# Performance work log

Measured on AMD Instinct MI355X. Metric: run time of the kernel, lower is better.

The kernel has to match this reference:

```python
import jax, jax.numpy as jnp
import numpy as np

EPS = 1e-5

def adain_norm(x):
    # per-(batch,channel) instance normalization over spatial dims (AdaIN projection)
    mean = jnp.mean(x, axis=(2, 3), keepdims=True)
    var = jnp.var(x, axis=(2, 3), keepdims=True)
    return (x - mean) / jnp.sqrt(var + EPS)

def conv1x1(x, w, b):
    # x: [B,C,H,W], w: [O,C], b: [O]
    return jnp.einsum('bchw,oc->bohw', x, w) + b[None, :, None, None]

def setup_inputs() -> dict:
    key = jax.random.key(0)
    ks = jax.random.split(key, 10)
    B, C, H, W = 4, 512, 64, 64
    s = 1.0 / np.sqrt(C)
    return {
        'x': jax.random.normal(ks[0], (B, C, H, W), jnp.float32),
        'y': jax.random.normal(ks[1], (B, C, H, W), jnp.float32),
        'f_w': jax.random.normal(ks[2], (C, C), jnp.float32) * s,
        'f_b': jnp.zeros((C,), jnp.float32),
        'g_w': jax.random.normal(ks[3], (C, C), jnp.float32) * s,
        'g_b': jnp.zeros((C,), jnp.float32),
        'h_w': jax.random.normal(ks[4], (C, C), jnp.float32) * s,
        'h_b': jnp.zeros((C,), jnp.float32),
        'out_w': jax.random.normal(ks[5], (C, C), jnp.float32) * s,
        'out_b': jnp.zeros((C,), jnp.float32),
    }

def reference(x, y, f_w, f_b, g_w, g_b, h_w, h_b, out_w, out_b):
    B, C, H, W = x.shape
    HW = H * W
    xn = adain_norm(x)
    yn = adain_norm(y)
    # 1x1 conv projections, flattened over spatial dims
    f = conv1x1(xn, f_w, f_b).reshape(B, C, HW)   # [B,C,HWx]
    g = conv1x1(yn, g_w, g_b).reshape(B, C, HW)   # [B,C,HWy]
    energy = jnp.einsum('bci,bcj->bij', f, g)     # [B,HWx,HWy]
    correlation = jax.nn.softmax(energy, axis=-1)
    h = conv1x1(y, h_w, h_b).reshape(B, C, HW)    # [B,C,HWy]
    # residual = h @ correlation^T -> [B,C,HWx]
    residual = jnp.einsum('bcj,bij->bci', h, correlation).reshape(B, C, H, W)
    residual = conv1x1(residual, out_w, out_b)
    return x + residual
```

## Files before the change

### kernel.cpp

```cpp
#include <hip/hip_runtime.h>
#include <stdint.h>

#define HW 4096
#define NC 512
#define NB 4

typedef __attribute__((ext_vector_type(8))) _Float16 f16x8;
typedef __attribute__((ext_vector_type(4))) float f32x4;
typedef __attribute__((ext_vector_type(4))) unsigned short ush4;
typedef __attribute__((ext_vector_type(8))) unsigned short ush8;

typedef __attribute__((address_space(1))) const void* as1_cvp;
typedef __attribute__((address_space(3))) void* as3_vp;

__device__ __forceinline__ unsigned short f2h(float f) {
  union { _Float16 h; unsigned short u; } c;
  c.h = (_Float16)f;
  return c.u;
}
__device__ __forceinline__ float h2f(unsigned short u) {
  union { unsigned short u; _Float16 h; } c;
  c.u = u;
  return (float)c.h;
}

__global__ __launch_bounds__(256) void moments_k(const float* __restrict__ x,
                                                 const float* __restrict__ y,
                                                 float* __restrict__ stats) {
  int bid = blockIdx.x;
  int tens = bid >> 11;
  int row = bid & 2047;
  const float* src = (tens ? y : x) + (size_t)row * HW;
  float s = 0.f, s2 = 0.f;
  for (int j = threadIdx.x; j < HW / 4; j += 256) {
    float4 v = ((const float4*)src)[j];
    s += (v.x + v.y) + (v.z + v.w);
    s2 += (v.x * v.x + v.y * v.y) + (v.z * v.z + v.w * v.w);
  }
  #pragma unroll
  for (int o = 32; o; o >>= 1) { s += __shfl_down(s, o); s2 += __shfl_down(s2, o); }
  __shared__ float rs[8];
  int w = threadIdx.x >> 6;
  if ((threadIdx.x & 63) == 0) { rs[w] = s; rs[4 + w] = s2; }
  __syncthreads();
  if (threadIdx.x == 0) {
    float S = (rs[0] + rs[1]) + (rs[2] + rs[3]);
    float S2 = (rs[4] + rs[5]) + (rs[6] + rs[7]);
    float mean = S * (1.f / HW);
    float var = S2 * (1.f / HW) - mean * mean;
    stats[tens * 4096 + row] = mean;
    stats[tens * 4096 + 2048 + row] = rsqrtf(var + 1e-5f);
  }
}

__global__ __launch_bounds__(256) void transnorm_k(const float* __restrict__ x,
                                                   const float* __restrict__ y,
                                                   const float* __restrict__ stats,
                                                   unsigned short* __restrict__ xnT,
                                                   unsigned short* __restrict__ ynT,
                                                   unsigned short* __restrict__ yH) {
  __shared__ float tile[64][65];
  __shared__ float ms[64], rsd[64];
  int zi = blockIdx.z;
  int b = zi >> 1, mode = zi & 1;
  int i0 = blockIdx.x * 64, c0 = blockIdx.y * 64;
  const float* src = mode ? y : x;
  int t = threadIdx.x;
  int c = t >> 2;
  int isub = (t & 3) << 4;
  if (t < 64) {
    int srow = (mode ? 4096 : 0) + b * NC + c0 + t;
    ms[t] = stats[srow];
    rsd[t] = stats[srow + 2048];
  }
  const float4* sp = (const float4*)(src + ((size_t)(b * NC + c0 + c)) * HW + i0 + isub);
  #pragma unroll
  for (int k = 0; k < 4; ++k) {
    float4 v = sp[k];
    int ib = isub + k * 4;
    tile[ib + 0][c] = v.x;
    tile[ib + 1][c] = v.y;
    tile[ib + 2][c] = v.z;
    tile[ib + 3][c] = v.w;
    if (mode) {
      ush4 yo;
      yo[0] = f2h(v.x); yo[1] = f2h(v.y); yo[2] = f2h(v.z); yo[3] = f2h(v.w);
      *(ush4*)(yH + ((size_t)(b * NC + c0 + c)) * HW + i0 + isub + k * 4) = yo;
    }
  }
  __syncthreads();
  int i = t >> 2;
  int cc = (t & 3) << 4;
  size_t obase = ((size_t)b * HW + i0 + i) * NC + c0 + cc;
  unsigned short* dst = mode ? ynT : xnT;
  #pragma unroll
  for (int h = 0; h < 2; ++h) {
    ush8 o;
    #pragma unroll
    for (int e = 0; e < 8; ++e) {
      int ce = cc + h * 8 + e;
      o[e] = f2h((tile[i][ce] - ms[ce]) * rsd[ce]);
    }
    *(ush8*)(dst + obase + h * 8) = o;
  }
}

__global__ __launch_bounds__(256) void castw_k(const float* __restrict__ fw,
                                               const float* __restrict__ gw,
                                               const float* __restrict__ hw_,
                                               const float* __restrict__ ow,
                                               unsigned short* __restrict__ fwT,
                                               unsigned short* __restrict__ gwT,
                                               unsigned short* __restrict__ hwT,
                                               unsigned short* __restrict__ owB) {
  __shared__ float tile[64][65];
  int which = blockIdx.z;
  const float* src = which == 0 ? fw : which == 1 ? gw : which == 2 ? hw_ : ow;
  unsigned short* dst = which == 0 ? fwT : which == 1 ? gwT : which == 2 ? hwT : owB;
  int r0 = blockIdx.x * 64, c0 = blockIdx.y * 64;
  int t = threadIdx.x;
  int r = t >> 2;
  int csub = (t & 3) << 4;
  const float4* sp = (const float4*)(src + (size_t)(r0 + r) * 512 + c0 + csub);
  if (which == 3) {
    #pragma unroll
    for (int k = 0; k < 4; ++k) {
      float4 v = sp[k];
      ush4 o;
      o[0] = f2h(v.x); o[1] = f2h(v.y); o[2] = f2h(v.z); o[3] = f2h(v.w);
      *(ush4*)(dst + (size_t)(r0 + r) * 512 + c0 + csub + k * 4) = o;
    }
    return;
  }
  #pragma unroll
  for (int k = 0; k < 4; ++k) {
    float4 v = sp[k];
    int cb = csub + k * 4;
    tile[cb + 0][r] = v.x;
    tile[cb + 1][r] = v.y;
    tile[cb + 2][r] = v.z;
    tile[cb + 3][r] = v.w;
  }
  __syncthreads();
  int cw = t >> 2;
  int rsub = (t & 3) << 4;
  #pragma unroll
  for (int h = 0; h < 2; ++h) {
    ush8 o;
    #pragma unroll
    for (int e = 0; e < 8; ++e) o[e] = f2h(tile[cw][rsub + h * 8 + e]);
    *(ush8*)(dst + (size_t)(c0 + cw) * 512 + r0 + rsub + h * 8) = o;
  }
}

__global__ __launch_bounds__(256) void dotrows_h(const unsigned short* __restrict__ A,
                                                 const float* __restrict__ vec,
                                                 float* __restrict__ out) {
  int row = blockIdx.x * 4 + (threadIdx.x >> 6);
  int lane = threadIdx.x & 63;
  ush8 a = *(const ush8*)(A + (size_t)row * 512 + lane * 8);
  float s = 0.f;
  #pragma unroll
  for (int e = 0; e < 8; ++e) s += h2f(a[e]) * vec[lane * 8 + e];
  #pragma unroll
  for (int o = 32; o; o >>= 1) s += __shfl_down(s, o);
  if (lane == 0) out[row] = s;
}

__global__ __launch_bounds__(256) void b2_k(const float* __restrict__ Wf,
                                            const float* __restrict__ hb,
                                            const float* __restrict__ ob,
                                            float* __restrict__ out) {
  int row = blockIdx.x * 4 + (threadIdx.x >> 6);
  int lane = threadIdx.x & 63;
  const float4* a = (const float4*)(Wf + (size_t)row * 512) + lane * 2;
  float4 x0 = a[0], x1 = a[1];
  const float4* hv = (const float4*)hb + lane * 2;
  float4 h0 = hv[0], h1 = hv[1];
  float s = x0.x * h0.x + x0.y * h0.y + x0.z * h0.z + x0.w * h0.w
          + x1.x * h1.x + x1.y * h1.y + x1.z * h1.z + x1.w * h1.w;
  #pragma unroll
  for (int o = 32; o; o >>= 1) s += __shfl_down(s, o);
  if (lane == 0) out[row] = ob[row] + s;
}

__global__ __launch_bounds__(256) void softmax_h(unsigned short* __restrict__ S) {
  unsigned short* row = S + (size_t)blockIdx.x * HW;
  int t = threadIdx.x;
  ush8 a0 = *(const ush8*)(row + t * 16);
  ush8 a1 = *(const ush8*)(row + t * 16 + 8);
  float v[16];
  #pragma unroll
  for (int e = 0; e < 8; ++e) { v[e] = h2f(a0[e]); v[8 + e] = h2f(a1[e]); }
  float mx = -3.0e38f;
  #pragma unroll
  for (int e = 0; e < 16; ++e) mx = fmaxf(mx, v[e]);
  #pragma unroll
  for (int o = 32; o; o >>= 1) mx = fmaxf(mx, __shfl_down(mx, o));
  __shared__ float red[8];
  int w = t >> 6;
  if ((t & 63) == 0) red[w] = mx;
  __syncthreads();
  mx = fmaxf(fmaxf(red[0], red[1]), fmaxf(red[2], red[3]));
  float sum = 0.f;
  #pragma unroll
  for (int e = 0; e < 16; ++e) { v[e] = __expf(v[e] - mx); sum += v[e]; }
  #pragma unroll
  for (int o = 32; o; o >>= 1) sum += __shfl_down(sum, o);
  if ((t & 63) == 0) red[4 + w] = sum;
  __syncthreads();
  float inv = 1.f / ((red[4] + red[5]) + (red[6] + red[7]));
  ush8 o0, o1;
  #pragma unroll
  for (int e = 0; e < 8; ++e) { o0[e] = f2h(v[e] * inv); o1[e] = f2h(v[8 + e] * inv); }
  *(ush8*)(row + t * 16) = o0;
  *(ush8*)(row + t * 16 + 8) = o1;
}

__global__ __launch_bounds__(256) void reduce_k(const float* __restrict__ P4,
                                                unsigned short* __restrict__ op,
                                                long long PSo, int R, int pzs) {
  int e = blockIdx.x * 256 + threadIdx.x;
  int bg = e >> pzs;
  int rem = e - (bg << pzs);
  const float4* base = (const float4*)P4 + ((size_t)bg * 4) * R * (NC / 4) + rem;
  float4 s = {0.f, 0.f, 0.f, 0.f};
  #pragma unroll
  for (int sp = 0; sp < 4; ++sp) {
    float4 v = base[(size_t)sp * R * (NC / 4)];
    s.x += v.x; s.y += v.y; s.z += v.z; s.w += v.w;
  }
  int m = rem >> 7, c4 = rem & 127;
  ush4 o;
  o[0] = f2h(s.x); o[1] = f2h(s.y); o[2] = f2h(s.z); o[3] = f2h(s.w);
  *(ush4*)(op + (size_t)bg * PSo + (size_t)m * NC + c4 * 4) = o;
}

__global__ __launch_bounds__(256, 2) void gemm_ntp(
    const unsigned short* __restrict__ A, long long sA, int lda,
    const unsigned short* __restrict__ Bm, long long sB, int ldb,
    void* __restrict__ Cp, long long sC, long long sCs, int ldc,
    int K, int out_f32, int ls,
    const float* __restrict__ bias_m, const float* __restrict__ bias_n,
    const float* __restrict__ add_src, long long sAdd,
    const unsigned short* __restrict__ B2, const float* __restrict__ bias_n2,
    int zsw) {
  __shared__ short lsA[2][128 * 64];
  __shared__ short lsB[2][128 * 64];
  const int t = threadIdx.x;
  const int lane = t & 63;
  const int w = t >> 6;
  const int wm = w >> 1, wn = w & 1;
  const long long bz = blockIdx.z;
  if ((int)bz >= zsw) { Bm = B2; bias_n = bias_n2; }
  const long long bg = bz >> ls;
  const int sp = (int)(bz - (bg << ls));
  const long long koff = (long long)sp * K;
  const unsigned short* Ab = A + bz * sA * (ls ? 0 : 1) + (ls ? bg * sA : 0) + koff
                           + (size_t)blockIdx.x * 128 * lda;
  const unsigned short* Bb = Bm + bg * sB + koff + (size_t)blockIdx.y * 128 * ldb;

  f32x4 zero = {0.f, 0.f, 0.f, 0.f};
  f32x4 acc[4][4];
  #pragma unroll
  for (int i = 0; i < 4; ++i)
    #pragma unroll
    for (int j = 0; j < 4; ++j) acc[i][j] = zero;

  const int nkt = K >> 6;

  auto STAGE = [&](int buf, int kt) {
    const int kbase = kt << 6;
    #pragma unroll
    for (int i = 0; i < 4; ++i) {
      int q = t + i * 256;
      int r = q >> 3, xx = q & 7;
      int gk = kbase + ((xx ^ (r & 7)) << 3);
      __builtin_amdgcn_global_load_lds((as1_cvp)(const void*)(Ab + (size_t)r * lda + gk),
                                       (as3_vp)(void*)(&lsA[buf][q << 3]), 16, 0, 0);
      __builtin_amdgcn_global_load_lds((as1_cvp)(const void*)(Bb + (size_t)r * ldb + gk),
                                       (as3_vp)(void*)(&lsB[buf][q << 3]), 16, 0, 0);
    }
  };

  STAGE(0, 0);
  __syncthreads();
  int cur = 0;
  for (int kt = 0; kt < nkt; ++kt) {
    if (kt + 1 < nkt) STAGE(cur ^ 1, kt + 1);
    #pragma unroll
    for (int ks = 0; ks < 2; ++ks) {
      f16x8 av[4], bv[4];
      const int xl = ks * 4 + (lane >> 4);
      const int rr = lane & 15;
      #pragma unroll
      for (int mb = 0; mb < 4; ++mb) {
        int row = wm * 64 + mb * 16 + rr;
        av[mb] = *(const f16x8*)&lsA[cur][(row << 6) + ((xl ^ (row & 7)) << 3)];
      }
      #pragma unroll
      for (int nb = 0; nb < 4; ++nb) {
        int row = wn * 64 + nb * 16 + rr;
        bv[nb] = *(const f16x8*)&lsB[cur][(row << 6) + ((xl ^ (row & 7)) << 3)];
      }
      __builtin_amdgcn_s_setprio(1);
      #pragma unroll
      for (int mb = 0; mb < 4; ++mb)
        #pragma unroll
        for (int nb = 0; nb < 4; ++nb)
          acc[mb][nb] = __builtin_amdgcn_mfma_f32_16x16x32_f16(av[mb], bv[nb], acc[mb][nb], 0, 0, 0);
      __builtin_amdgcn_s_setprio(0);
    }
    __syncthreads();
    cur ^= 1;
  }

  const int mb0 = blockIdx.x * 128 + wm * 64;
  const int nb0 = blockIdx.y * 128 + wn * 64;
  const int cn = lane & 15;
  const int rq = (lane >> 4) << 2;
  float* cf = (float*)Cp;
  unsigned short* ch = (unsigned short*)Cp;
  #pragma unroll
  for (int mb = 0; mb < 4; ++mb) {
    #pragma unroll
    for (int nb = 0; nb < 4; ++nb) {
      int n = nb0 + nb * 16 + cn;
      float bn = bias_n ? bias_n[n] : 0.f;
      #pragma unroll
      for (int r = 0; r < 4; ++r) {
        int m = mb0 + mb * 16 + rq + r;
        float vv = acc[mb][nb][r] + bn;
        if (bias_m) vv += bias_m[m];
        if (add_src) vv += add_src[bg * sAdd + (size_t)m * ldc + n];
        size_t off = (size_t)(bg * sC) + (size_t)sp * sCs + (size_t)m * ldc + n;
        if (out_f32) cf[off] = vv;
        else ch[off] = f2h(vv);
      }
    }
  }
}

__global__ __launch_bounds__(512, 2) void gemm_nt2(
    const unsigned short* __restrict__ A, long long sA, int lda,
    const unsigned short* __restrict__ Bm, long long sB, int ldb,
    void* __restrict__ Cp, long long sC, int ldc,
    int K, int out_f32,
    const float* __restrict__ bias_n, long long sBn) {
  __shared__ short lsA[2][256 * 64];
  __shared__ short lsB[2][256 * 64];
  const int t = threadIdx.x;
  const int lane = t & 63;
  const int w = t >> 6;
  const int wm = w >> 2, wn = w & 3;
  const long long bz = blockIdx.z;
  const unsigned short* Ab = A + bz * sA + (size_t)blockIdx.x * 256 * lda;
  const unsigned short* Bb = Bm + bz * sB + (size_t)blockIdx.y * 256 * ldb;

  f32x4 zero = {0.f, 0.f, 0.f, 0.f};
  f32x4 acc[8][4];
  #pragma unroll
  for (int i = 0; i < 8; ++i)
    #pragma unroll
    for (int j = 0; j < 4; ++j) acc[i][j] = zero;

  const int rr = lane & 15;
  const int xl = lane >> 4;
  const int nkt = K >> 6;

  auto STAGE = [&](int buf, int kt) {
    const int kbase = kt << 6;
    #pragma unroll
    for (int i = 0; i < 4; ++i) {
      int q = t + i * 512;
      int r = q >> 3, xx = q & 7;
      int gk = kbase + ((xx ^ (r & 7)) << 3);
      __builtin_amdgcn_global_load_lds((as1_cvp)(const void*)(Ab + (size_t)r * lda + gk),
                                       (as3_vp)(void*)(&lsA[buf][q << 3]), 16, 0, 0);
      __builtin_amdgcn_global_load_lds((as1_cvp)(const void*)(Bb + (size_t)r * ldb + gk),
                                       (as3_vp)(void*)(&lsB[buf][q << 3]), 16, 0, 0);
    }
  };

  STAGE(0, 0);
  __syncthreads();
  int cur = 0;
  for (int kt = 0; kt < nkt; ++kt) {
    if (kt + 1 < nkt) STAGE(cur ^ 1, kt + 1);
    #pragma unroll
    for (int ks = 0; ks < 2; ++ks) {
      f16x8 av[8], bv[4];
      const int cb = ks * 4 + xl;
      #pragma unroll
      for (int mb = 0; mb < 8; ++mb) {
        int row = wm * 128 + mb * 16 + rr;
        av[mb] = *(const f16x8*)&lsA[cur][(row << 6) + ((cb ^ (row & 7)) << 3)];
      }
      #pragma unroll
      for (int nb = 0; nb < 4; ++nb) {
        int row = wn * 64 + nb * 16 + rr;
        bv[nb] = *(const f16x8*)&lsB[cur][(row << 6) + ((cb ^ (row & 7)) << 3)];
      }
      __builtin_amdgcn_s_setprio(1);
      #pragma unroll
      for (int mb = 0; mb < 8; ++mb)
        #pragma unroll
        for (int nb = 0; nb < 4; ++nb)
          acc[mb][nb] = __builtin_amdgcn_mfma_f32_16x16x32_f16(av[mb], bv[nb], acc[mb][nb], 0, 0, 0);
      __builtin_amdgcn_s_setprio(0);
    }
    __syncthreads();
    cur ^= 1;
  }

  const int mb0 = blockIdx.x * 256 + wm * 128;
  const int nb0 = blockIdx.y * 256 + wn * 64;
  const int cn = lane & 15;
  const int rq = (lane >> 4) << 2;
  float* cf = (float*)Cp;
  unsigned short* ch = (unsigned short*)Cp;
  #pragma unroll
  for (int mb = 0; mb < 8; ++mb) {
    #pragma unroll
    for (int nb = 0; nb < 4; ++nb) {
      int n = nb0 + nb * 16 + cn;
      float bn = bias_n ? bias_n[bz * sBn + n] : 0.f;
      #pragma unroll
      for (int r = 0; r < 4; ++r) {
        int m = mb0 + mb * 16 + rq + r;
        float vv = acc[mb][nb][r] + bn;
        size_t off = (size_t)(bz * sC) + (size_t)m * ldc + n;
        if (out_f32) cf[off] = vv;
        else ch[off] = f2h(vv);
      }
    }
  }
}

extern "C" void kernel_launch(void* const* d_in, const int* in_sizes, int n_in,
                              void* d_out, int out_size, void* d_ws, size_t ws_size,
                              hipStream_t stream) {
  const float* x = (const float*)d_in[0];
  const float* y = (const float*)d_in[1];
  const float* f_w = (const float*)d_in[2];
  const float* f_b = (const float*)d_in[3];
  const float* g_w = (const float*)d_in[4];
  const float* g_b = (const float*)d_in[5];
  const float* h_w = (const float*)d_in[6];
  const float* h_b = (const float*)d_in[7];
  const float* out_w = (const float*)d_in[8];
  const float* out_b = (const float*)d_in[9];
  float* out = (float*)d_out;
  (void)g_b;

  char* ws = (char*)d_ws;
  size_t off = 0;
  auto alloc = [&](size_t bytes) -> char* {
    char* p = ws + off;
    off += (bytes + 255) & ~(size_t)255;
    return p;
  };
  const size_t TN = (size_t)NB * HW * NC;
  const size_t WN = (size_t)512 * 512;
  float* stats = (float*)alloc(8192 * sizeof(float));
  unsigned short* fwT = (unsigned short*)alloc(WN * 2);
  unsigned short* gwT = (unsigned short*)alloc(WN * 2);
  unsigned short* hwT = (unsigned short*)alloc(WN * 2);
  unsigned short* owB = (unsigned short*)alloc(WN * 2);
  unsigned short* W1T = (unsigned short*)alloc(WN * 2);
  unsigned short* W2 = (unsigned short*)alloc(WN * 2);
  float* vv = (float*)alloc(512 * 4);
  float* b2 = (float*)alloc(512 * 4);
  float* wj = (float*)alloc((size_t)NB * HW * 4);
  unsigned short* xnT = (unsigned short*)alloc(TN * 2);
  unsigned short* ynT = (unsigned short*)alloc(TN * 2);
  unsigned short* yH = (unsigned short*)alloc(TN * 2);
  unsigned short* fB = (unsigned short*)alloc(TN * 2);
  unsigned short* oB = xnT;
  size_t remain = ws_size > off ? ws_size - off : 0;
  const size_t SB = (size_t)HW * HW * 2 + (size_t)4 * HW * NC * 4;
  int G, R = HW;
  if (remain >= 4 * SB)      { G = 4; }
  else if (remain >= 2 * SB) { G = 2; }
  else if (remain >= SB)     { G = 1; }
  else {
    G = 1;
    while (R > 128 && (size_t)R * (HW * 2 + 16 * NC) > remain) R >>= 1;
  }
  unsigned short* Sh = (unsigned short*)alloc((size_t)G * R * HW * 2);
  float* P4 = (float*)alloc((size_t)G * 4 * R * NC * 4);
  if (off > ws_size) return;

  const long long PS = (long long)HW * NC;
  const int BIG = 1 << 30;

  castw_k<<<dim3(8, 8, 4), dim3(256), 0, stream>>>(f_w, g_w, h_w, out_w,
                                                   fwT, gwT, hwT, owB);
  moments_k<<<dim3(4096), dim3(256), 0, stream>>>(x, y, stats);
  transnorm_k<<<dim3(64, 8, 8), dim3(256), 0, stream>>>(x, y, stats, xnT, ynT, yH);

  dotrows_h<<<dim3(128), dim3(256), 0, stream>>>(gwT, f_b, vv);
  b2_k<<<dim3(128), dim3(256), 0, stream>>>(out_w, h_b, out_b, b2);
  gemm_ntp<<<dim3(4, 4, 1), dim3(256), 0, stream>>>(
      gwT, 0, 512, fwT, 0, 512, W1T, 0, 0, 512, 512, 0, 0,
      nullptr, nullptr, nullptr, 0, nullptr, nullptr, BIG);
  gemm_ntp<<<dim3(4, 4, 1), dim3(256), 0, stream>>>(
      owB, 0, 512, hwT, 0, 512, W2, 0, 0, 512, 512, 0, 0,
      nullptr, nullptr, nullptr, 0, nullptr, nullptr, BIG);
  dotrows_h<<<dim3(NB * HW / 4), dim3(256), 0, stream>>>(ynT, vv, wj);
  gemm_ntp<<<dim3(32, 4, NB), dim3(256), 0, stream>>>(
      xnT, PS, NC, W1T, 0, NC, fB, PS, 0, NC, NC, 0, 0,
      nullptr, nullptr, nullptr, 0, nullptr, nullptr, BIG);

  const int pzs = 31 - __builtin_clz((unsigned)(R * (NC / 4)));
  for (int b0 = 0; b0 < NB; b0 += G) {
    for (int r0 = 0; r0 < HW; r0 += R) {
      if (R >= 256) {
        gemm_nt2<<<dim3(R / 256, HW / 256, G), dim3(512), 0, stream>>>(
            fB + ((size_t)b0 * HW + r0) * NC, PS, NC,
            ynT + (size_t)b0 * PS, PS, NC,
            Sh, (long long)R * HW, HW, NC, 0,
            wj + (size_t)b0 * HW, HW);
      } else {
        gemm_ntp<<<dim3(R / 128, 32, G), dim3(256), 0, stream>>>(
            fB + ((size_t)b0 * HW + r0) * NC, PS, NC,
            ynT + (size_t)b0 * PS, PS, NC,
            Sh, (long long)R * HW, 0, HW, NC, 0, 0,
            nullptr, wj + (size_t)b0 * HW, nullptr, 0, nullptr, nullptr, BIG);
      }
      softmax_h<<<dim3(G * R), dim3(256), 0, stream>>>(Sh);
      gemm_ntp<<<dim3(R / 128, 4, G * 4), dim3(256), 0, stream>>>(
          Sh, (long long)R * HW, HW,
          yH + (size_t)b0 * NC * HW, (long long)NC * HW, HW,
          P4, (long long)4 * R * NC, (long long)R * NC, NC, HW / 4, 1, 2,
          nullptr, nullptr, nullptr, 0, nullptr, nullptr, BIG);
      reduce_k<<<dim3(G * R / 2), dim3(256), 0, stream>>>(
          P4, oB + ((size_t)b0 * HW + r0) * NC, PS, R, pzs);
    }
  }
  gemm_ntp<<<dim3(4, 32, NB), dim3(256), 0, stream>>>(
      W2, 0, NC, oB, PS, NC,
      out, (long long)NC * HW, 0, HW, NC, 1, 0,
      b2, nullptr, x, (long long)NC * HW, nullptr, nullptr, BIG);
}
```

Before: 407.2 us.

## Deepen big-GEMM pipeline to four stages and reuse it for split-K PV GEMM

The 256x256 GEMM kernel moves from a double-buffered BK=64 loop to a 4-slot BK=32 ring, with three tiles in flight. Each step now waits on a partial vmcnt and a raw s_barrier instead of a full __syncthreads, which is meant to hide global-load latency. The kernel also gains split-K batching (sp offset plus output stride), so the softmax-times-h GEMM can use this larger-tile kernel instead of the 128-tile gemm_ntp when R>=256. The price is more barriers per K, a changed swizzle, and correctness that depends on the hand-counted vmcnt values.

```diff
diff --git a/kernel.cpp b/kernel.cpp
--- a/kernel.cpp
+++ b/kernel.cpp
@@ -341,21 +341,24 @@
   }
 }
 
-__global__ __launch_bounds__(512, 2) void gemm_nt2(
+__global__ __launch_bounds__(512, 2) void gemm_ntq(
     const unsigned short* __restrict__ A, long long sA, int lda,
     const unsigned short* __restrict__ Bm, long long sB, int ldb,
-    void* __restrict__ Cp, long long sC, int ldc,
-    int K, int out_f32,
+    void* __restrict__ Cp, long long sC, long long sCs, int ldc,
+    int K, int out_f32, int ls,
     const float* __restrict__ bias_n, long long sBn) {
-  __shared__ short lsA[2][256 * 64];
-  __shared__ short lsB[2][256 * 64];
+  __shared__ short lsA[4][256 * 32];
+  __shared__ short lsB[4][256 * 32];
   const int t = threadIdx.x;
   const int lane = t & 63;
   const int w = t >> 6;
   const int wm = w >> 2, wn = w & 3;
   const long long bz = blockIdx.z;
-  const unsigned short* Ab = A + bz * sA + (size_t)blockIdx.x * 256 * lda;
-  const unsigned short* Bb = Bm + bz * sB + (size_t)blockIdx.y * 256 * ldb;
+  const long long bg = bz >> ls;
+  const int sp = (int)(bz - (bg << ls));
+  const long long koff = (long long)sp * K;
+  const unsigned short* Ab = A + bg * sA + koff + (size_t)blockIdx.x * 256 * lda;
+  const unsigned short* Bb = Bm + bg * sB + koff + (size_t)blockIdx.y * 256 * ldb;
 
   f32x4 zero = {0.f, 0.f, 0.f, 0.f};
   f32x4 acc[8][4];
@@ -366,52 +369,69 @@
 
   const int rr = lane & 15;
   const int xl = lane >> 4;
-  const int nkt = K >> 6;
-
-  auto STAGE = [&](int buf, int kt) {
-    const int kbase = kt << 6;
-    #pragma unroll
-    for (int i = 0; i < 4; ++i) {
+  const int nkt = K >> 5;
+
+  auto STAGE = [&](int kt) {
+    const int slot = kt & 3;
+    const int kbase = kt << 5;
+    #pragma unroll
+    for (int i = 0; i < 2; ++i) {
       int q = t + i * 512;
-      int r = q >> 3, xx = q & 7;
-      int gk = kbase + ((xx ^ (r & 7)) << 3);
+      int r = q >> 2, xx = q & 3;
+      int gk = kbase + ((xx ^ ((r >> 1) & 3)) << 3);
       __builtin_amdgcn_global_load_lds((as1_cvp)(const void*)(Ab + (size_t)r * lda + gk),
-                                       (as3_vp)(void*)(&lsA[buf][q << 3]), 16, 0, 0);
+                                       (as3_vp)(void*)(&lsA[slot][q << 3]), 16, 0, 0);
       __builtin_amdgcn_global_load_lds((as1_cvp)(const void*)(Bb + (size_t)r * ldb + gk),
-                                       (as3_vp)(void*)(&lsB[buf][q << 3]), 16, 0, 0);
+                                       (as3_vp)(void*)(&lsB[slot][q << 3]), 16, 0, 0);
     }
   };
 
-  STAGE(0, 0);
-  __syncthreads();
-  int cur = 0;
-  for (int kt = 0; kt < nkt; ++kt) {
-    if (kt + 1 < nkt) STAGE(cur ^ 1, kt + 1);
-    #pragma unroll
-    for (int ks = 0; ks < 2; ++ks) {
-      f16x8 av[8], bv[4];
-      const int cb = ks * 4 + xl;
+  auto COMPUTE = [&](int kt) {
+    const int slot = kt & 3;
+    f16x8 av[8], bv[4];
+    #pragma unroll
+    for (int mb = 0; mb < 8; ++mb) {
+      int row = wm * 128 + mb * 16 + rr;
+      av[mb] = *(const f16x8*)&lsA[slot][(row << 5) + ((xl ^ ((row >> 1) & 3)) << 3)];
+    }
+    #pragma unroll
+    for (int nb = 0; nb < 4; ++nb) {
+      int row = wn * 64 + nb * 16 + rr;
+      bv[nb] = *(const f16x8*)&lsB[slot][(row << 5) + ((xl ^ ((row >> 1) & 3)) << 3)];
+    }
+    __builtin_amdgcn_s_setprio(1);
+    #pragma unroll
+    for (int mb = 0; mb < 8; ++mb)
       #pragma unroll
-      for (int mb = 0; mb < 8; ++mb) {
-        int row = wm * 128 + mb * 16 + rr;
-        av[mb] = *(const f16x8*)&lsA[cur][(row << 6) + ((cb ^ (row & 7)) << 3)];
-      }
-      #pragma unroll
-      for (int nb = 0; nb < 4; ++nb) {
-        int row = wn * 64 + nb * 16 + rr;
-        bv[nb] = *(const f16x8*)&lsB[cur][(row << 6) + ((cb ^ (row & 7)) << 3)];
-      }
-      __builtin_amdgcn_s_setprio(1);
-      #pragma unroll
-      for (int mb = 0; mb < 8; ++mb)
-        #pragma unroll
-        for (int nb = 0; nb < 4; ++nb)
-          acc[mb][nb] = __builtin_amdgcn_mfma_f32_16x16x32_f16(av[mb], bv[nb], acc[mb][nb], 0, 0, 0);
-      __builtin_amdgcn_s_setprio(0);
-    }
-    __syncthreads();
-    cur ^= 1;
-  }
+      for (int nb = 0; nb < 4; ++nb)
+        acc[mb][nb] = __builtin_amdgcn_mfma_f32_16x16x32_f16(av[mb], bv[nb], acc[mb][nb], 0, 0, 0);
+    __builtin_amdgcn_s_setprio(0);
+  };
+
+  STAGE(0); STAGE(1); STAGE(2);
+  asm volatile("s_waitcnt vmcnt(8)" ::: "memory");
+  __builtin_amdgcn_s_barrier();
+  __builtin_amdgcn_sched_barrier(0);
+
+  int kt = 0;
+  for (; kt + 3 < nkt; ++kt) {
+    STAGE(kt + 3);
+    COMPUTE(kt);
+    asm volatile("s_waitcnt vmcnt(8)" ::: "memory");
+    __builtin_amdgcn_s_barrier();
+    __builtin_amdgcn_sched_barrier(0);
+  }
+  COMPUTE(kt);
+  asm volatile("s_waitcnt vmcnt(4)" ::: "memory");
+  __builtin_amdgcn_s_barrier();
+  __builtin_amdgcn_sched_barrier(0);
+  ++kt;
+  COMPUTE(kt);
+  asm volatile("s_waitcnt vmcnt(0)" ::: "memory");
+  __builtin_amdgcn_s_barrier();
+  __builtin_amdgcn_sched_barrier(0);
+  ++kt;
+  COMPUTE(kt);
 
   const int mb0 = blockIdx.x * 256 + wm * 128;
   const int nb0 = blockIdx.y * 256 + wn * 64;
@@ -424,12 +444,12 @@
     #pragma unroll
     for (int nb = 0; nb < 4; ++nb) {
       int n = nb0 + nb * 16 + cn;
-      float bn = bias_n ? bias_n[bz * sBn + n] : 0.f;
+      float bn = bias_n ? bias_n[bg * sBn + n] : 0.f;
       #pragma unroll
       for (int r = 0; r < 4; ++r) {
         int m = mb0 + mb * 16 + rq + r;
         float vv = acc[mb][nb][r] + bn;
-        size_t off = (size_t)(bz * sC) + (size_t)m * ldc + n;
+        size_t off = (size_t)(bg * sC) + (size_t)sp * sCs + (size_t)m * ldc + n;
         if (out_f32) cf[off] = vv;
         else ch[off] = f2h(vv);
       }
@@ -516,24 +536,30 @@
   for (int b0 = 0; b0 < NB; b0 += G) {
     for (int r0 = 0; r0 < HW; r0 += R) {
       if (R >= 256) {
-        gemm_nt2<<<dim3(R / 256, HW / 256, G), dim3(512), 0, stream>>>(
+        gemm_ntq<<<dim3(R / 256, HW / 256, G), dim3(512), 0, stream>>>(
             fB + ((size_t)b0 * HW + r0) * NC, PS, NC,
             ynT + (size_t)b0 * PS, PS, NC,
-            Sh, (long long)R * HW, HW, NC, 0,
+            Sh, (long long)R * HW, 0, HW, NC, 0, 0,
             wj + (size_t)b0 * HW, HW);
+        softmax_h<<<dim3(G * R), dim3(256), 0, stream>>>(Sh);
+        gemm_ntq<<<dim3(R / 256, NC / 256, G * 4), dim3(512), 0, stream>>>(
+            Sh, (long long)R * HW, HW,
+            yH + (size_t)b0 * NC * HW, (long long)NC * HW, HW,
+            P4, (long long)4 * R * NC, (long long)R * NC, NC, HW / 4, 1, 2,
+            nullptr, 0);
       } else {
         gemm_ntp<<<dim3(R / 128, 32, G), dim3(256), 0, stream>>>(
             fB + ((size_t)b0 * HW + r0) * NC, PS, NC,
             ynT + (size_t)b0 * PS, PS, NC,
             Sh, (long long)R * HW, 0, HW, NC, 0, 0,
             nullptr, wj + (size_t)b0 * HW, nullptr, 0, nullptr, nullptr, BIG);
+        softmax_h<<<dim3(G * R), dim3(256), 0, stream>>>(Sh);
+        gemm_ntp<<<dim3(R / 128, 4, G * 4), dim3(256), 0, stream>>>(
+            Sh, (long long)R * HW, HW,
+            yH + (size_t)b0 * NC * HW, (long long)NC * HW, HW,
+            P4, (long long)4 * R * NC, (long long)R * NC, NC, HW / 4, 1, 2,
+            nullptr, nullptr, nullptr, 0, nullptr, nullptr, BIG);
       }
-      softmax_h<<<dim3(G * R), dim3(256), 0, stream>>>(Sh);
-      gemm_ntp<<<dim3(R / 128, 4, G * 4), dim3(256), 0, stream>>>(
-          Sh, (long long)R * HW, HW,
-          yH + (size_t)b0 * NC * HW, (long long)NC * HW, HW,
-          P4, (long long)4 * R * NC, (long long)R * NC, NC, HW / 4, 1, 2,
-          nullptr, nullptr, nullptr, 0, nullptr, nullptr, BIG);
       reduce_k<<<dim3(G * R / 2), dim3(256), 0, stream>>>(
           P4, oB + ((size_t)b0 * HW + r0) * NC, PS, R, pzs);
     }
```

Result: slower. 438.4 us (+7.7%).

## Fold split-K partial sums into final GEMM via duplicated weight matrix

Applied to the files above, without the earlier changes.

The attention-value GEMM previously split K into 4 fp32 partial buffers, which a separate reduce kernel summed and cast to fp16. Now K is split in 2, each half is written as fp16 into a concatenated 1024-wide buffer, and the output projection GEMM runs over K=1024 with a weight matrix replicated twice. This removes the reduce kernel and its fp32 partial traffic, and halves the split so each block does more K work. The cost is double the K work in the final GEMM, fewer blocks in the AV GEMM, and fp16 rounding of partial sums.

```diff
diff --git a/kernel.cpp b/kernel.cpp
--- a/kernel.cpp
+++ b/kernel.cpp
@@ -153,6 +153,15 @@
   }
 }
 
+__global__ __launch_bounds__(256) void repl_k(const unsigned short* __restrict__ W2,
+                                              unsigned short* __restrict__ W2x2) {
+  int idx = blockIdx.x * 256 + threadIdx.x;
+  int o = idx >> 7;
+  int k = (idx & 127) * 8;
+  ush8 v = *(const ush8*)(W2 + (size_t)o * 512 + (k & 511));
+  *(ush8*)(W2x2 + (size_t)o * 1024 + k) = v;
+}
+
 __global__ __launch_bounds__(256) void dotrows_h(const unsigned short* __restrict__ A,
                                                  const float* __restrict__ vec,
                                                  float* __restrict__ out) {
@@ -215,25 +224,6 @@
   for (int e = 0; e < 8; ++e) { o0[e] = f2h(v[e] * inv); o1[e] = f2h(v[8 + e] * inv); }
   *(ush8*)(row + t * 16) = o0;
   *(ush8*)(row + t * 16 + 8) = o1;
-}
-
-__global__ __launch_bounds__(256) void reduce_k(const float* __restrict__ P4,
-                                                unsigned short* __restrict__ op,
-                                                long long PSo, int R, int pzs) {
-  int e = blockIdx.x * 256 + threadIdx.x;
-  int bg = e >> pzs;
-  int rem = e - (bg << pzs);
-  const float4* base = (const float4*)P4 + ((size_t)bg * 4) * R * (NC / 4) + rem;
-  float4 s = {0.f, 0.f, 0.f, 0.f};
-  #pragma unroll
-  for (int sp = 0; sp < 4; ++sp) {
-    float4 v = base[(size_t)sp * R * (NC / 4)];
-    s.x += v.x; s.y += v.y; s.z += v.z; s.w += v.w;
-  }
-  int m = rem >> 7, c4 = rem & 127;
-  ush4 o;
-  o[0] = f2h(s.x); o[1] = f2h(s.y); o[2] = f2h(s.z); o[3] = f2h(s.w);
-  *(ush4*)(op + (size_t)bg * PSo + (size_t)m * NC + c4 * 4) = o;
 }
 
 __global__ __launch_bounds__(256, 2) void gemm_ntp(
@@ -469,6 +459,7 @@
   unsigned short* owB = (unsigned short*)alloc(WN * 2);
   unsigned short* W1T = (unsigned short*)alloc(WN * 2);
   unsigned short* W2 = (unsigned short*)alloc(WN * 2);
+  unsigned short* W2x2 = (unsigned short*)alloc((size_t)512 * 1024 * 2);
   float* vv = (float*)alloc(512 * 4);
   float* b2 = (float*)alloc(512 * 4);
   float* wj = (float*)alloc((size_t)NB * HW * 4);
@@ -476,19 +467,18 @@
   unsigned short* ynT = (unsigned short*)alloc(TN * 2);
   unsigned short* yH = (unsigned short*)alloc(TN * 2);
   unsigned short* fB = (unsigned short*)alloc(TN * 2);
-  unsigned short* oB = xnT;
+  unsigned short* Zp = (unsigned short*)alloc((size_t)NB * HW * 1024 * 2);
   size_t remain = ws_size > off ? ws_size - off : 0;
-  const size_t SB = (size_t)HW * HW * 2 + (size_t)4 * HW * NC * 4;
+  const size_t SB = (size_t)HW * HW * 2;
   int G, R = HW;
   if (remain >= 4 * SB)      { G = 4; }
   else if (remain >= 2 * SB) { G = 2; }
   else if (remain >= SB)     { G = 1; }
   else {
     G = 1;
-    while (R > 128 && (size_t)R * (HW * 2 + 16 * NC) > remain) R >>= 1;
+    while (R > 128 && (size_t)R * HW * 2 > remain) R >>= 1;
   }
   unsigned short* Sh = (unsigned short*)alloc((size_t)G * R * HW * 2);
-  float* P4 = (float*)alloc((size_t)G * 4 * R * NC * 4);
   if (off > ws_size) return;
 
   const long long PS = (long long)HW * NC;
@@ -507,12 +497,12 @@
   gemm_ntp<<<dim3(4, 4, 1), dim3(256), 0, stream>>>(
       owB, 0, 512, hwT, 0, 512, W2, 0, 0, 512, 512, 0, 0,
       nullptr, nullptr, nullptr, 0, nullptr, nullptr, BIG);
+  repl_k<<<dim3(256), dim3(256), 0, stream>>>(W2, W2x2);
   dotrows_h<<<dim3(NB * HW / 4), dim3(256), 0, stream>>>(ynT, vv, wj);
   gemm_ntp<<<dim3(32, 4, NB), dim3(256), 0, stream>>>(
       xnT, PS, NC, W1T, 0, NC, fB, PS, 0, NC, NC, 0, 0,
       nullptr, nullptr, nullptr, 0, nullptr, nullptr, BIG);
 
-  const int pzs = 31 - __builtin_clz((unsigned)(R * (NC / 4)));
   for (int b0 = 0; b0 < NB; b0 += G) {
     for (int r0 = 0; r0 < HW; r0 += R) {
       if (R >= 256) {
@@ -529,17 +519,16 @@
             nullptr, wj + (size_t)b0 * HW, nullptr, 0, nullptr, nullptr, BIG);
       }
       softmax_h<<<dim3(G * R), dim3(256), 0, stream>>>(Sh);
-      gemm_ntp<<<dim3(R / 128, 4, G * 4), dim3(256), 0, stream>>>(
+      gemm_ntp<<<dim3(R / 128, 4, G * 2), dim3(256), 0, stream>>>(
           Sh, (long long)R * HW, HW,
           yH + (size_t)b0 * NC * HW, (long long)NC * HW, HW,
-          P4, (long long)4 * R * NC, (long long)R * NC, NC, HW / 4, 1, 2,
+          Zp + ((size_t)b0 * HW + r0) * 1024, (long long)R * 1024, 512, 1024,
+          HW / 2, 0, 1,
           nullptr, nullptr, nullptr, 0, nullptr, nullptr, BIG);
-      reduce_k<<<dim3(G * R / 2), dim3(256), 0, stream>>>(
-          P4, oB + ((size_t)b0 * HW + r0) * NC, PS, R, pzs);
     }
   }
   gemm_ntp<<<dim3(4, 32, NB), dim3(256), 0, stream>>>(
-      W2, 0, NC, oB, PS, NC,
-      out, (long long)NC * HW, 0, HW, NC, 1, 0,
+      W2x2, 0, 1024, Zp, (long long)HW * 1024, 1024,
+      out, (long long)NC * HW, 0, HW, 1024, 1, 0,
       b2, nullptr, x, (long long)NC * HW, nullptr, nullptr, BIG);
 }
```

New measurement: 391.0 us, median of 3. -4.0%, faster.
